# Optimization experiments

Hardware: AMD Instinct MI355X
Metric: run time of the kernel (lower is better)

## Reference

```python
import jax, jax.numpy as jnp
import numpy as np

EPS = 1e-5
NUM_HEADS = 8
TOP_K = 4

def _ln(x, s, b):
    m = x.mean(-1, keepdims=True)
    v = ((x - m) ** 2).mean(-1, keepdims=True)
    return (x - m) / jnp.sqrt(v + EPS) * s + b

def _mha(x, wq, bq, wk, bk, wv, bv, wo, bo):
    B, S, D = x.shape
    dh = D // NUM_HEADS
    q = (x @ wq + bq).reshape(B, S, NUM_HEADS, dh)
    k = (x @ wk + bk).reshape(B, S, NUM_HEADS, dh)
    v = (x @ wv + bv).reshape(B, S, NUM_HEADS, dh)
    att = jnp.einsum('bqhd,bkhd->bhqk', q, k) / np.sqrt(dh).astype(x.dtype)
    a = jax.nn.softmax(att, axis=-1)
    o = jnp.einsum('bhqk,bkhd->bqhd', a, v).reshape(B, S, D)
    return o @ wo + bo

def _moe(x, rd, ru, w1, b1, w2, b2, ws1, bs1, ws2, bs2):
    B, S, D = x.shape
    N = B * S
    E = ru.shape[-1]
    t = x.reshape(N, D)
    scores = (t @ rd) @ ru                       # [N,E] low-rank router
    probs = jax.nn.softmax(scores, axis=-1)
    tv, ti = jax.lax.top_k(probs, TOP_K)          # [N,K]
    tw = tv / tv.sum(-1, keepdims=True)           # renormalized gate weights
    oh = jax.nn.one_hot(ti, E, dtype=t.dtype)     # [N,K,E]
    gates = (oh * tw[..., None]).sum(1)           # sparse [N,E] combine weights
    h = jax.nn.gelu(jnp.einsum('nd,edh->enh', t, w1) + b1[:, None, :])
    eo = jnp.einsum('enh,ehd->end', h, w2) + b2[:, None, :]
    routed = jnp.einsum('end,ne->nd', eo, gates)
    shared = jax.nn.gelu(t @ ws1 + bs1) @ ws2 + bs2
    out = (routed + shared).reshape(B, S, D)
    # aux losses: load-balance + router z-loss
    f = oh.sum(1).mean(0)                         # mean assignments per expert
    P = probs.mean(0)
    lb = (E / TOP_K) * jnp.sum(f * P)
    z = jnp.mean(jax.nn.logsumexp(scores, axis=-1) ** 2)
    return out, lb, z

def reference(x, ln1_s, ln1_b, ln2_s, ln2_b, wq, bq, wk, bk, wv, bv, wo, bo,
              router_down, router_up, w1, b1, w2, b2, ws1, bs1, ws2, bs2, fn_s, fn_b):
    L = wq.shape[0]
    lbs, zs = [], []
    for l in range(L):
        x = x + _mha(_ln(x, ln1_s[l], ln1_b[l]), wq[l], bq[l], wk[l], bk[l],
                     wv[l], bv[l], wo[l], bo[l])
        moe_out, lb, z = _moe(_ln(x, ln2_s[l], ln2_b[l]), router_down[l], router_up[l],
                              w1[l], b1[l], w2[l], b2[l], ws1[l], bs1[l], ws2[l], bs2[l])
        x = x + moe_out
        lbs.append(lb)
        zs.append(z)
    x = _ln(x, fn_s, fn_b)
    return x, jnp.stack(lbs), jnp.stack(zs)

def setup_inputs() -> dict:
    key = jax.random.key(0)
    ks = jax.random.split(key, 16)
    L, D, E, R, H, HS, B, S = 2, 512, 32, 64, 512, 4096, 4, 1024
    w = 0.02  # init scale for weights
    return {
        'x': jax.random.normal(ks[0], (B, S, D), jnp.float32),
        'ln1_s': jnp.ones((L, D)), 'ln1_b': jnp.zeros((L, D)),
        'ln2_s': jnp.ones((L, D)), 'ln2_b': jnp.zeros((L, D)),
        'wq': jax.random.normal(ks[1], (L, D, D)) * w, 'bq': jnp.zeros((L, D)),
        'wk': jax.random.normal(ks[2], (L, D, D)) * w, 'bk': jnp.zeros((L, D)),
        'wv': jax.random.normal(ks[3], (L, D, D)) * w, 'bv': jnp.zeros((L, D)),
        'wo': jax.random.normal(ks[4], (L, D, D)) * w, 'bo': jnp.zeros((L, D)),
        'router_down': jax.random.normal(ks[5], (L, D, R)) * w,
        'router_up': jax.random.normal(ks[6], (L, R, E)) * w,
        'w1': jax.random.normal(ks[7], (L, E, D, H)) * w, 'b1': jnp.zeros((L, E, H)),
        'w2': jax.random.normal(ks[8], (L, E, H, D)) * w, 'b2': jnp.zeros((L, E, D)),
        'ws1': jax.random.normal(ks[9], (L, D, HS)) * w, 'bs1': jnp.zeros((L, HS)),
        'ws2': jax.random.normal(ks[10], (L, HS, D)) * w, 'bs2': jnp.zeros((L, D)),
        'fn_s': jnp.ones((D,)), 'fn_b': jnp.zeros((D,)),
    }
```

## Files before the change

kernel.cpp:

```cpp
#include <hip/hip_runtime.h>
#include <math.h>

#define NTOK    4096
#define DMODEL  512
#define NEXP    32
#define RRANK   64
#define HEXP    512
#define HSHARED 4096
#define SEQ     1024
#define BATCH   4
#define NHEAD   8
#define TOPK    4
#define NLAYER  2
#define QBLK    64
#define KBLK    64
#define MAXTILE 160
#define DDU     262144

typedef __attribute__((ext_vector_type(8))) short bf16x8;
typedef __attribute__((ext_vector_type(4))) float f32x4;

__device__ __forceinline__ float gelu_f(float x) {
    float t = tanhf(0.7978845608028654f * (x + 0.044715f * x * x * x));
    return 0.5f * x * (1.f + t);
}
__device__ __forceinline__ unsigned short f2bf(float f) {
    unsigned int u = __float_as_uint(f);
    u += 0x7FFFu + ((u >> 16) & 1u);
    return (unsigned short)(u >> 16);
}
__device__ __forceinline__ float bf2f(unsigned short u) {
    return __uint_as_float((unsigned int)u << 16);
}
__device__ __forceinline__ void gl_lds16(const void* g, void* l) {
    __builtin_amdgcn_global_load_lds(
        (const __attribute__((address_space(1))) void*)g,
        (__attribute__((address_space(3))) void*)l, 16, 0, 0);
}

__device__ __forceinline__ void ln_body(const float* x, const float* s, const float* b,
                                        unsigned short* outb, int rowblk) {
    int wave = threadIdx.x >> 6, lane = threadIdx.x & 63;
    int row = rowblk * 4 + wave;
    const float* xr = x + (size_t)row * DMODEL;
    float v[8];
    float sum = 0.f;
#pragma unroll
    for (int i = 0; i < 8; i++) { v[i] = xr[lane + i * 64]; sum += v[i]; }
#pragma unroll
    for (int o = 32; o; o >>= 1) sum += __shfl_xor(sum, o);
    float m = sum * (1.f / DMODEL);
    float vs = 0.f;
#pragma unroll
    for (int i = 0; i < 8; i++) { float d = v[i] - m; vs += d * d; }
#pragma unroll
    for (int o = 32; o; o >>= 1) vs += __shfl_xor(vs, o);
    float rstd = rsqrtf(vs * (1.f / DMODEL) + 1e-5f);
#pragma unroll
    for (int i = 0; i < 8; i++) {
        int c = lane + i * 64;
        outb[(size_t)row * DMODEL + c] = f2bf((v[i] - m) * rstd * s[c] + b[c]);
    }
}

template <int SK, bool MOE, int MODE, bool ROUTER = false>
__global__ __launch_bounds__(256) void reduceln_kernel(
    const float* __restrict__ pbuf, const float* __restrict__ bias,
    const unsigned short* __restrict__ eogb, const float* __restrict__ topw,
    const int* __restrict__ pos, float* __restrict__ xb,
    const float* __restrict__ s, const float* __restrict__ b,
    float* __restrict__ outf, unsigned short* __restrict__ outb,
    const float* __restrict__ rdru, float* __restrict__ rsc) {
    int wave = threadIdx.x >> 6, lane = threadIdx.x & 63;
    int row = blockIdx.x * 4 + wave;
    int cb = lane * 8;
    size_t base = (size_t)row * DMODEL + cb;
    float v[8];
    {
        float4 a0 = *(const float4*)(xb + base);
        float4 a1 = *(const float4*)(xb + base + 4);
        float4 b0 = *(const float4*)(bias + cb);
        float4 b1 = *(const float4*)(bias + cb + 4);
        v[0] = a0.x + b0.x; v[1] = a0.y + b0.y; v[2] = a0.z + b0.z; v[3] = a0.w + b0.w;
        v[4] = a1.x + b1.x; v[5] = a1.y + b1.y; v[6] = a1.z + b1.z; v[7] = a1.w + b1.w;
    }
#pragma unroll
    for (int sk = 0; sk < SK; sk++) {
        const float* p = pbuf + (size_t)sk * NTOK * DMODEL + base;
        float4 p0 = *(const float4*)p;
        float4 p1 = *(const float4*)(p + 4);
        v[0] += p0.x; v[1] += p0.y; v[2] += p0.z; v[3] += p0.w;
        v[4] += p1.x; v[5] += p1.y; v[6] += p1.z; v[7] += p1.w;
    }
    if (MOE) {
#pragma unroll
        for (int k = 0; k < TOPK; k++) {
            float w = topw[row * TOPK + k];
            bf16x8 e = *(const bf16x8*)(eogb + (size_t)pos[row * TOPK + k] * DMODEL + cb);
#pragma unroll
            for (int i = 0; i < 8; i++) v[i] += w * bf2f((unsigned short)e[i]);
        }
    }
    *(float4*)(xb + base) = make_float4(v[0], v[1], v[2], v[3]);
    *(float4*)(xb + base + 4) = make_float4(v[4], v[5], v[6], v[7]);
    float sum = 0.f;
#pragma unroll
    for (int i = 0; i < 8; i++) sum += v[i];
#pragma unroll
    for (int o = 32; o; o >>= 1) sum += __shfl_xor(sum, o);
    float m = sum * (1.f / DMODEL);
    float vs = 0.f;
#pragma unroll
    for (int i = 0; i < 8; i++) { float d = v[i] - m; vs += d * d; }
#pragma unroll
    for (int o = 32; o; o >>= 1) vs += __shfl_xor(vs, o);
    float rstd = rsqrtf(vs * (1.f / DMODEL) + 1e-5f);
    float rr[8];
#pragma unroll
    for (int i = 0; i < 8; i++) {
        int c = cb + i;
        rr[i] = (v[i] - m) * rstd * s[c] + b[c];
        if (MODE != 1) outf[(size_t)row * DMODEL + c] = rr[i];
        if (MODE != 0) outb[(size_t)row * DMODEL + c] = f2bf(rr[i]);
    }
    if (ROUTER) {
        float sc[NEXP];
#pragma unroll
        for (int e = 0; e < NEXP; e++) sc[e] = 0.f;
#pragma unroll
        for (int i = 0; i < 8; i++) {
            const float4* rp = (const float4*)(rdru + (size_t)(cb + i) * NEXP);
            float rv = rr[i];
#pragma unroll
            for (int e4 = 0; e4 < 8; e4++) {
                float4 q = rp[e4];
                sc[e4 * 4 + 0] += rv * q.x;
                sc[e4 * 4 + 1] += rv * q.y;
                sc[e4 * 4 + 2] += rv * q.z;
                sc[e4 * 4 + 3] += rv * q.w;
            }
        }
#pragma unroll
        for (int e = 0; e < NEXP; e++) {
#pragma unroll
            for (int o = 32; o; o >>= 1) sc[e] += __shfl_xor(sc[e], o);
        }
        if (lane == 0) {
            float* rp = rsc + (size_t)row * NEXP;
#pragma unroll
            for (int e = 0; e < NEXP; e++) rp[e] = sc[e];
        }
    }
}

__device__ __forceinline__ void wt_tile_body(char* ldsraw, const float* src,
                                             unsigned short* dst, int K, int N,
                                             int tx, int ty) {
    float (*tbuf)[68] = (float(*)[68])ldsraw;
    int tid = threadIdx.x;
    int k0 = ty * 64, n0 = tx * 64;
    int r = tid >> 2, cb4 = (tid & 3) * 4;
#pragma unroll
    for (int i = 0; i < 4; i++)
        *(float4*)&tbuf[r][cb4 + i * 16] = *(const float4*)(src + (size_t)(k0 + r) * N + n0 + cb4 + i * 16);
    __syncthreads();
    int g = tid & 7, nr = tid >> 3;
#pragma unroll
    for (int i = 0; i < 2; i++) {
        int n = nr + i * 32;
        bf16x8 v;
#pragma unroll
        for (int j = 0; j < 8; j++) v[j] = (short)f2bf(tbuf[g * 8 + j][n]);
        *(bf16x8*)(dst + (size_t)(n0 + n) * K + k0 + g * 8) = v;
    }
}

__device__ __forceinline__ void rdru_tile_body(char* ldsraw, const float* A,
                                               const float* W, float* C, int m0) {
    float (*Asf)[68] = (float(*)[68])ldsraw;
    float (*Wsf)[68] = (float(*)[68])(ldsraw + 4352);
    int tid = threadIdx.x;
    int ml = tid >> 2, kl = (tid & 3) << 2;
    const float* aptr = A + (size_t)(m0 + ml) * RRANK + kl;
    int kr = tid >> 4, nc = (tid & 15) << 2;
    bool wvalid = nc < NEXP;
    const float* wptr = W + (size_t)kr * NEXP + nc;
    int tm = (tid >> 4) << 2, tn = (tid & 15) << 2;
    float acc[4][4] = {{0.f}};
    for (int k0 = 0; k0 < RRANK; k0 += 16) {
        float4 av = *(const float4*)(aptr + k0);
        float4 wv = make_float4(0.f, 0.f, 0.f, 0.f);
        if (wvalid) wv = *(const float4*)(wptr + (size_t)k0 * NEXP);
        Asf[kl + 0][ml] = av.x; Asf[kl + 1][ml] = av.y;
        Asf[kl + 2][ml] = av.z; Asf[kl + 3][ml] = av.w;
        *(float4*)&Wsf[kr][nc] = wv;
        __syncthreads();
#pragma unroll
        for (int kk = 0; kk < 16; kk++) {
            float4 a4 = *(const float4*)&Asf[kk][tm];
            float4 w4 = *(const float4*)&Wsf[kk][tn];
            acc[0][0] += a4.x * w4.x; acc[0][1] += a4.x * w4.y; acc[0][2] += a4.x * w4.z; acc[0][3] += a4.x * w4.w;
            acc[1][0] += a4.y * w4.x; acc[1][1] += a4.y * w4.y; acc[1][2] += a4.y * w4.z; acc[1][3] += a4.y * w4.w;
            acc[2][0] += a4.z * w4.x; acc[2][1] += a4.z * w4.y; acc[2][2] += a4.z * w4.z; acc[2][3] += a4.z * w4.w;
            acc[3][0] += a4.w * w4.x; acc[3][1] += a4.w * w4.y; acc[3][2] += a4.w * w4.z; acc[3][3] += a4.w * w4.w;
        }
        __syncthreads();
    }
#pragma unroll
    for (int i = 0; i < 4; i++) {
        float* crow = C + (size_t)(m0 + tm + i) * NEXP;
#pragma unroll
        for (int j = 0; j < 4; j++) {
            int nn = tn + j;
            if (nn < NEXP) crow[nn] = acc[i][j];
        }
    }
}

__global__ __launch_bounds__(256) void prep0_kernel(
    const float* __restrict__ wq, const float* __restrict__ wk, const float* __restrict__ wv,
    const float* __restrict__ bq, const float* __restrict__ bk, const float* __restrict__ bv,
    unsigned short* __restrict__ wqkvt, float* __restrict__ bqkv, int* __restrict__ stats,
    const float* __restrict__ rdw, const float* __restrict__ ruw, float* __restrict__ rdru,
    const float* __restrict__ xb, const float* __restrict__ ln1_s, const float* __restrict__ ln1_b,
    unsigned short* __restrict__ hb) {
    __shared__ char lds[17408];
    int bkid = blockIdx.x;
    int tid = threadIdx.x;
    if (bkid < 192) {
        int w = bkid >> 6, t = bkid & 63;
        const float* src = (w == 0) ? wq : (w == 1 ? wk : wv);
        wt_tile_body(lds, src, wqkvt + (size_t)w * DDU, 512, 512, t & 7, t >> 3);
    } else if (bkid < 198) {
        int i = (bkid - 192) * 256 + tid;
        float val = (i < 512) ? bq[i] : (i < 1024 ? bk[i - 512] : bv[i - 1024]);
        bqkv[i] = val;
        if (i < 160) stats[i] = 0;
    } else if (bkid < 206) {
        rdru_tile_body(lds, rdw, ruw, rdru, (bkid - 198) * 64);
    } else {
        ln_body(xb, ln1_s, ln1_b, hb, bkid - 206);
    }
}

__global__ __launch_bounds__(256) void vtr_kernel(const unsigned short* __restrict__ QKV,
                                                  unsigned short* __restrict__ Vt) {
    int st = blockIdx.x, hh = blockIdx.y, bb = blockIdx.z;
    __shared__ unsigned short t[64][72];
    int r = threadIdx.x >> 3, g = threadIdx.x & 7;
#pragma unroll
    for (int i = 0; i < 2; i++) {
        int row = r + i * 32;
        bf16x8 v = *(const bf16x8*)(QKV + (size_t)(bb * SEQ + st * 64 + row) * 1536 + 1024 + hh * 64 + g * 8);
        *(bf16x8*)&t[row][g * 8] = v;
    }
    __syncthreads();
#pragma unroll
    for (int i = 0; i < 2; i++) {
        int d = r + i * 32;
        bf16x8 v;
#pragma unroll
        for (int j = 0; j < 8; j++) v[j] = (short)t[g * 8 + j][d];
        *(bf16x8*)(Vt + (size_t)((bb * NHEAD + hh) * 64 + d) * SEQ + st * 64 + g * 8) = v;
    }
}

template <bool GELU, bool GATHER, bool EXPERT, bool OUTBF16, int SK>
__device__ __forceinline__ void gemm_body(
    char* asb, char* bsb,
    unsigned int rb, unsigned int gx, unsigned int tot, int zidx,
    const unsigned short* Ab, const unsigned short* Wt,
    const float* bias, void* Cvoid, int M, int Nn, int Kk,
    const int* rowmap, const int* cntp, const int* offp, const int* tinfo) {
    constexpr int RS  = 128;
    constexpr int CH  = 8;
    constexpr int RPI = 8;
    constexpr int AIW = 4;
    constexpr int BIW = 2;
    unsigned int lg = (rb & 7) * (tot >> 3) + (rb >> 3);
    unsigned int bx = lg % gx;
    unsigned int by = lg / gx;
    int n0 = bx * 64;
    int m0;
    size_t cbase = 0;
    int kbeg = 0, kend = Kk;
    if (EXPERT) {
        int t = by;
        if (t >= tinfo[0]) return;
        int e = tinfo[1 + 2 * t];
        m0 = tinfo[2 + 2 * t];
        M = cntp[e];
        Wt += (size_t)e * Nn * Kk;
        bias += (size_t)e * Nn;
        int oe = offp[e];
        cbase = (size_t)oe * Nn;
        if (GATHER) rowmap += oe;
        else Ab += (size_t)oe * Kk;
    } else {
        m0 = by * 128;
    }
    if (SK > 1) {
        int chunk = Kk / SK;
        kbeg = zidx * chunk;
        kend = kbeg + chunk;
        cbase = (size_t)zidx * M * Nn;
    }
    int tid = threadIdx.x;
    int wave = tid >> 6, lane = tid & 63;
    int wm = wave >> 1, wn = wave & 1;
    int l15 = lane & 15, l16 = lane >> 4;
    int c16 = lane & (CH - 1);
    int ro  = lane / CH;

    const char* aptr[AIW];
    const char* bptr[BIW];
#pragma unroll
    for (int j = 0; j < AIW; j++) {
        int rloc = j * RPI + ro;
        int row = wave * 32 + rloc;
        int grow = m0 + row;
        int arow = GATHER ? rowmap[grow] : grow;
        int srcoff = ((c16 ^ (rloc & (CH - 1))) << 4);
        aptr[j] = (const char*)Ab + (((size_t)arow * Kk) << 1) + srcoff;
    }
#pragma unroll
    for (int j = 0; j < BIW; j++) {
        int rloc = j * RPI + ro;
        int row = wave * 16 + rloc;
        int srcoff = ((c16 ^ (rloc & (CH - 1))) << 4);
        bptr[j] = (const char*)Wt + (((size_t)(n0 + row) * Kk) << 1) + srcoff;
    }

    f32x4 acc[4][2];
#pragma unroll
    for (int m = 0; m < 4; m++)
#pragma unroll
        for (int n = 0; n < 2; n++)
#pragma unroll
            for (int j = 0; j < 4; j++) acc[m][n][j] = 0.f;

    for (int k0 = kbeg; k0 < kend; k0 += 64) {
        size_t kb = (size_t)k0 << 1;
#pragma unroll
        for (int j = 0; j < AIW; j++) gl_lds16(aptr[j] + kb, asb + wave * 32 * RS + j * 1024);
#pragma unroll
        for (int j = 0; j < BIW; j++) gl_lds16(bptr[j] + kb, bsb + wave * 16 * RS + j * 1024);
        __syncthreads();
#pragma unroll
        for (int kk = 0; kk < 2; kk++) {
            int k8 = kk * 4 + l16;
            bf16x8 a[4], b[2];
#pragma unroll
            for (int m = 0; m < 4; m++) {
                int row = wm * 64 + m * 16 + l15;
                a[m] = *(const bf16x8*)(asb + row * RS + ((k8 * 16) ^ ((row & (CH - 1)) << 4)));
            }
#pragma unroll
            for (int n = 0; n < 2; n++) {
                int row = wn * 32 + n * 16 + l15;
                b[n] = *(const bf16x8*)(bsb + row * RS + ((k8 * 16) ^ ((row & (CH - 1)) << 4)));
            }
#pragma unroll
            for (int m = 0; m < 4; m++)
#pragma unroll
                for (int n = 0; n < 2; n++)
                    acc[m][n] = __builtin_amdgcn_mfma_f32_16x16x32_bf16(a[m], b[n], acc[m][n], 0, 0, 0);
        }
        __syncthreads();
    }

#pragma unroll
    for (int m = 0; m < 4; m++) {
#pragma unroll
        for (int n = 0; n < 2; n++) {
            int col = n0 + wn * 32 + n * 16 + l15;
            float bv = (SK == 1 && bias) ? bias[col] : 0.f;
#pragma unroll
            for (int j = 0; j < 4; j++) {
                int row = m0 + wm * 64 + m * 16 + l16 * 4 + j;
                if (row >= M) continue;
                float val = acc[m][n][j] + bv;
                if (SK == 1 && GELU) val = gelu_f(val);
                if (SK == 1 && OUTBF16)
                    ((unsigned short*)Cvoid)[cbase + (size_t)row * Nn + col] = f2bf(val);
                else
                    ((float*)Cvoid)[cbase + (size_t)row * Nn + col] = val;
            }
        }
    }
}

template <int RIDER>
__global__ __launch_bounds__(256, 2) void qkv_kernel(
    const unsigned short* __restrict__ hb, const unsigned short* __restrict__ wqkvt,
    const float* __restrict__ bqkv, unsigned short* __restrict__ qkv_bf,
    const float* __restrict__ srcA, const float* __restrict__ srcB,
    unsigned short* __restrict__ dstA, unsigned short* __restrict__ dstB,
    int* __restrict__ stats) {
    __shared__ char lds[24576];
    unsigned int bid = blockIdx.x;
    if (bid < 768) {
        gemm_body<false, false, false, true, 1>(
            lds, lds + 16384, bid, 24, 768, 0,
            hb, wqkvt, bqkv, qkv_bf, NTOK, 1536, DMODEL, nullptr, nullptr, nullptr, nullptr);
    } else if (RIDER == 0) {
        int t = bid - 768;
        wt_tile_body(lds, srcA, dstA, 512, 512, t & 7, t >> 3);
    } else {
        unsigned int eb = bid - 768;
        if (eb < 2048) {
            int e = eb >> 6, tt = eb & 63;
            wt_tile_body(lds, srcA + (size_t)e * DDU, dstA + (size_t)e * DDU,
                         512, 512, tt & 7, tt >> 3);
        } else if (eb < 2560) {
            int t = eb - 2048;
            wt_tile_body(lds, srcB, dstB, 4096, 512, t & 7, t >> 3);
        } else {
            if (threadIdx.x < 160) stats[threadIdx.x] = 0;
        }
    }
}

__device__ __forceinline__ void attn_body(char* lds, unsigned int bid,
                                          const unsigned short* QKV,
                                          const unsigned short* Vt,
                                          unsigned short* O) {
    int qt = bid & 15, hh = (bid >> 4) & 7, bb = bid >> 7;
    char* Qs = lds;
    char* Ks = lds + 8192;
    char* Vs = lds + 16384;
    char* Ps = lds + 24576;
    int tid = threadIdx.x;
    int w = tid >> 6, l = tid & 63;
    int l15 = l & 15, l16 = l >> 4;

    {
        int r = tid >> 3, g = tid & 7;
        const unsigned short* qbase = QKV + (size_t)(bb * SEQ + qt * QBLK) * 1536 + hh * 64;
#pragma unroll
        for (int i = 0; i < 2; i++) {
            int row = r + i * 32;
            bf16x8 v = *(const bf16x8*)(qbase + (size_t)row * 1536 + g * 8);
            *(bf16x8*)(Qs + row * 128 + ((g * 16) ^ ((row & 7) << 4))) = v;
        }
    }
    f32x4 accO[4];
#pragma unroll
    for (int n = 0; n < 4; n++)
#pragma unroll
        for (int j = 0; j < 4; j++) accO[n][j] = 0.f;
    float m_r[4] = {-1e30f, -1e30f, -1e30f, -1e30f};
    float l_r[4] = {0.f, 0.f, 0.f, 0.f};

    const unsigned short* kbase = QKV + (size_t)(bb * SEQ) * 1536 + 512 + hh * 64;
    const unsigned short* vbase = Vt + (size_t)((bb * NHEAD + hh) * 64) * SEQ;

    for (int kt = 0; kt < SEQ / KBLK; kt++) {
        __syncthreads();
        {
            int r = tid >> 3, g = tid & 7;
#pragma unroll
            for (int i = 0; i < 2; i++) {
                int row = r + i * 32;
                bf16x8 kv = *(const bf16x8*)(kbase + (size_t)(kt * KBLK + row) * 1536 + g * 8);
                *(bf16x8*)(Ks + row * 128 + ((g * 16) ^ ((row & 7) << 4))) = kv;
                bf16x8 vv = *(const bf16x8*)(vbase + (size_t)row * SEQ + kt * KBLK + g * 8);
                *(bf16x8*)(Vs + row * 128 + ((g * 16) ^ ((row & 7) << 4))) = vv;
            }
        }
        __syncthreads();
        f32x4 s_acc[4];
#pragma unroll
        for (int n = 0; n < 4; n++)
#pragma unroll
            for (int j = 0; j < 4; j++) s_acc[n][j] = 0.f;
#pragma unroll
        for (int st = 0; st < 2; st++) {
            int kb = st * 64 + l16 * 16;
            int qrow = w * 16 + l15;
            bf16x8 a = *(const bf16x8*)(Qs + qrow * 128 + (kb ^ ((qrow & 7) << 4)));
#pragma unroll
            for (int n = 0; n < 4; n++) {
                int kr = n * 16 + l15;
                bf16x8 b = *(const bf16x8*)(Ks + kr * 128 + (kb ^ ((kr & 7) << 4)));
                s_acc[n] = __builtin_amdgcn_mfma_f32_16x16x32_bf16(a, b, s_acc[n], 0, 0, 0);
            }
        }
        char* pw = Ps + w * 2048;
#pragma unroll
        for (int j = 0; j < 4; j++) {
            float s0 = s_acc[0][j] * 0.125f, s1 = s_acc[1][j] * 0.125f;
            float s2 = s_acc[2][j] * 0.125f, s3 = s_acc[3][j] * 0.125f;
            float tmax = fmaxf(fmaxf(s0, s1), fmaxf(s2, s3));
#pragma unroll
            for (int o = 1; o < 16; o <<= 1) tmax = fmaxf(tmax, __shfl_xor(tmax, o));
            float mnew = fmaxf(m_r[j], tmax);
            float resc = __expf(m_r[j] - mnew);
            float p0 = __expf(s0 - mnew), p1 = __expf(s1 - mnew);
            float p2 = __expf(s2 - mnew), p3 = __expf(s3 - mnew);
            float ps = p0 + p1 + p2 + p3;
#pragma unroll
            for (int o = 1; o < 16; o <<= 1) ps += __shfl_xor(ps, o);
            l_r[j] = l_r[j] * resc + ps;
            m_r[j] = mnew;
            accO[0][j] *= resc; accO[1][j] *= resc;
            accO[2][j] *= resc; accO[3][j] *= resc;
            int prow = l16 * 4 + j;
            int sw = (prow & 7) << 4;
            *(unsigned short*)(pw + prow * 128 + ((2 * l15) ^ sw)) = f2bf(p0);
            *(unsigned short*)(pw + prow * 128 + ((2 * l15 + 32) ^ sw)) = f2bf(p1);
            *(unsigned short*)(pw + prow * 128 + ((2 * l15 + 64) ^ sw)) = f2bf(p2);
            *(unsigned short*)(pw + prow * 128 + ((2 * l15 + 96) ^ sw)) = f2bf(p3);
        }
#pragma unroll
        for (int st = 0; st < 2; st++) {
            int kb = st * 64 + l16 * 16;
            bf16x8 pa = *(const bf16x8*)(pw + l15 * 128 + (kb ^ ((l15 & 7) << 4)));
#pragma unroll
            for (int n = 0; n < 4; n++) {
                int vr = n * 16 + l15;
                bf16x8 vb = *(const bf16x8*)(Vs + vr * 128 + (kb ^ ((vr & 7) << 4)));
                accO[n] = __builtin_amdgcn_mfma_f32_16x16x32_bf16(pa, vb, accO[n], 0, 0, 0);
            }
        }
    }
    unsigned short* obase = O + (size_t)(bb * SEQ + qt * QBLK + w * 16) * DMODEL + hh * 64;
#pragma unroll
    for (int j = 0; j < 4; j++) {
        float inv = 1.f / l_r[j];
        int row = l16 * 4 + j;
#pragma unroll
        for (int n = 0; n < 4; n++)
            obase[(size_t)row * DMODEL + n * 16 + l15] = f2bf(accO[n][j] * inv);
    }
}

template <int RIDER>
__global__ __launch_bounds__(256, 2) void attn_kernel(
    const unsigned short* __restrict__ QKV, const unsigned short* __restrict__ Vt,
    unsigned short* __restrict__ O,
    const float* __restrict__ w1src, const float* __restrict__ ws1src,
    unsigned short* __restrict__ w1t, unsigned short* __restrict__ ws1t) {
    __shared__ char lds[32768];
    unsigned int bid = blockIdx.x;
    if (bid < 512) {
        attn_body(lds, bid, QKV, Vt, O);
    } else if (RIDER == 0) {
        unsigned int eb = bid - 512;
        if (eb < 2048) {
            int e = eb >> 6, tt = eb & 63;
            wt_tile_body(lds, w1src + (size_t)e * DDU, w1t + (size_t)e * DDU,
                         512, 512, tt & 7, tt >> 3);
        } else {
            int t = eb - 2048;
            wt_tile_body(lds, ws1src, ws1t, 512, 4096, t & 63, t >> 6);
        }
    }
}

template <int RIDER>
__global__ __launch_bounds__(256, 2) void op_kernel(
    const unsigned short* __restrict__ t1b, const unsigned short* __restrict__ wot,
    float* __restrict__ pbuf,
    const float* __restrict__ w2src, const float* __restrict__ ws2src,
    unsigned short* __restrict__ w2t, unsigned short* __restrict__ ws2t) {
    __shared__ char lds[24576];
    unsigned int bid = blockIdx.x;
    if (bid < 512) {
        gemm_body<false, false, false, false, 2>(
            lds, lds + 16384, bid & 255, 8, 256, bid >> 8,
            t1b, wot, nullptr, pbuf, NTOK, DMODEL, DMODEL, nullptr, nullptr, nullptr, nullptr);
    } else if (RIDER == 0) {
        unsigned int eb = bid - 512;
        if (eb < 2048) {
            int e = eb >> 6, tt = eb & 63;
            wt_tile_body(lds, w2src + (size_t)e * DDU, w2t + (size_t)e * DDU,
                         512, 512, tt & 7, tt >> 3);
        } else {
            int t = eb - 2048;
            wt_tile_body(lds, ws2src, ws2t, 4096, 512, t & 7, t >> 3);
        }
    }
}

__global__ __launch_bounds__(256, 2) void mlp1_kernel(
    const unsigned short* __restrict__ hb,
    const unsigned short* __restrict__ ws1t, const float* __restrict__ bs1,
    unsigned short* __restrict__ hidb,
    const unsigned short* __restrict__ w1t, const float* __restrict__ b1,
    unsigned short* __restrict__ ehid,
    const int* __restrict__ perm, const int* __restrict__ cnt,
    const int* __restrict__ poff, const int* __restrict__ tinfo,
    const float* __restrict__ nwq, const float* __restrict__ nwk,
    const float* __restrict__ nwv, const float* __restrict__ nwo,
    const float* __restrict__ nbq, const float* __restrict__ nbk, const float* __restrict__ nbv,
    unsigned short* __restrict__ wqkvt, unsigned short* __restrict__ wot,
    float* __restrict__ bqkv,
    const float* __restrict__ nrdw, const float* __restrict__ nruw, float* __restrict__ rdru) {
    __shared__ char lds[24576];
    unsigned int bid = blockIdx.x;
    if (bid < 2048) {
        gemm_body<true, false, false, true, 1>(
            lds, lds + 16384, bid, 64, 2048, 0,
            hb, ws1t, bs1, hidb, NTOK, HSHARED, DMODEL, nullptr, nullptr, nullptr, nullptr);
    } else if (bid < 3328) {
        gemm_body<true, true, true, true, 1>(
            lds, lds + 16384, bid - 2048, 8, 1280, 0,
            hb, w1t, b1, ehid, 0, HEXP, DMODEL, perm, cnt, poff, tinfo);
    } else {
        unsigned int eb = bid - 3328;
        if (eb < 256) {
            int w = eb >> 6, t = eb & 63;
            const float* src; unsigned short* dst;
            if (w == 0)      { src = nwq; dst = wqkvt; }
            else if (w == 1) { src = nwk; dst = wqkvt + DDU; }
            else if (w == 2) { src = nwv; dst = wqkvt + 2 * (size_t)DDU; }
            else             { src = nwo; dst = wot; }
            wt_tile_body(lds, src, dst, 512, 512, t & 7, t >> 3);
        } else if (eb < 262) {
            int i = (eb - 256) * 256 + threadIdx.x;
            float val = (i < 512) ? nbq[i] : (i < 1024 ? nbk[i - 512] : nbv[i - 1024]);
            bqkv[i] = val;
        } else {
            rdru_tile_body(lds, nrdw, nruw, rdru, (eb - 262) * 64);
        }
    }
}

__global__ __launch_bounds__(256, 2) void mlp2_kernel(
    const unsigned short* __restrict__ hidb,
    const unsigned short* __restrict__ ws2t, float* __restrict__ pbuf,
    const unsigned short* __restrict__ ehid,
    const unsigned short* __restrict__ w2t, const float* __restrict__ b2,
    unsigned short* __restrict__ eogb,
    const int* __restrict__ cnt, const int* __restrict__ poff,
    const int* __restrict__ tinfo,
    const float* __restrict__ nw1, const float* __restrict__ nws1,
    unsigned short* __restrict__ w1t, unsigned short* __restrict__ ws1t) {
    __shared__ char lds[24576];
    unsigned int bid = blockIdx.x;
    if (bid < 1024) {
        int zidx = bid >> 8;
        gemm_body<false, false, false, false, 4>(
            lds, lds + 16384, bid & 255, 8, 256, zidx,
            hidb, ws2t, nullptr, pbuf, NTOK, DMODEL, HSHARED, nullptr, nullptr, nullptr, nullptr);
    } else if (bid < 2304) {
        gemm_body<false, false, true, true, 1>(
            lds, lds + 16384, bid - 1024, 8, 1280, 0,
            ehid, w2t, b2, eogb, 0, DMODEL, HEXP, nullptr, cnt, poff, tinfo);
    } else {
        unsigned int eb = bid - 2304;
        if (eb < 2048) {
            int e = eb >> 6, tt = eb & 63;
            wt_tile_body(lds, nw1 + (size_t)e * DDU, w1t + (size_t)e * DDU,
                         512, 512, tt & 7, tt >> 3);
        } else {
            int t = eb - 2048;
            wt_tile_body(lds, nws1, ws1t, 512, 4096, t & 63, t >> 6);
        }
    }
}

__global__ __launch_bounds__(256) void router_topk(const float* __restrict__ rsc,
                                                   float* __restrict__ topw,
                                                   int* __restrict__ topi,
                                                   int* __restrict__ cnt,
                                                   float* __restrict__ sumP,
                                                   float* __restrict__ zacc,
                                                   int* __restrict__ done,
                                                   int* __restrict__ poff,
                                                   int* __restrict__ tinfo,
                                                   int* __restrict__ perm,
                                                   float* __restrict__ out_aux, int l) {
    __shared__ float wP[4][NEXP];
    __shared__ int wC[4][NEXP];
    __shared__ float wZ[4];
    __shared__ int amLast;
    int tid = threadIdx.x;
    int wv = tid >> 6, lane = tid & 63;
    int n = blockIdx.x * 256 + tid;
    float sc[NEXP];
    float mx = -1e30f;
#pragma unroll
    for (int e = 0; e < NEXP; e++) { sc[e] = rsc[n * NEXP + e]; mx = fmaxf(mx, sc[e]); }
    float se = 0.f;
#pragma unroll
    for (int e = 0; e < NEXP; e++) { sc[e] = expf(sc[e] - mx); se += sc[e]; }
    float invse = 1.f / se;
    float lse = mx + logf(se);
    float z = lse * lse;
#pragma unroll
    for (int o = 32; o; o >>= 1) z += __shfl_xor(z, o);
    if (lane == 0) wZ[wv] = z;
#pragma unroll
    for (int e = 0; e < NEXP; e++) {
        float pv = sc[e] * invse;
#pragma unroll
        for (int o = 32; o; o >>= 1) pv += __shfl_xor(pv, o);
        if (lane == 0) wP[wv][e] = pv;
    }
    float tv[TOPK]; int ti[TOPK];
#pragma unroll
    for (int k = 0; k < TOPK; k++) {
        float best = -1.f; int bi = 0;
#pragma unroll
        for (int e = 0; e < NEXP; e++) {
            if (sc[e] > best) { best = sc[e]; bi = e; }
        }
        tv[k] = best * invse; ti[k] = bi; sc[bi] = -1.f;
    }
    float s4 = tv[0] + tv[1] + tv[2] + tv[3];
#pragma unroll
    for (int k = 0; k < TOPK; k++) {
        topw[n * TOPK + k] = tv[k] / s4;
        topi[n * TOPK + k] = ti[k];
    }
#pragma unroll
    for (int e = 0; e < NEXP; e++) {
        unsigned long long b0 = __ballot(ti[0] == e);
        unsigned long long b1 = __ballot(ti[1] == e);
        unsigned long long b2 = __ballot(ti[2] == e);
        unsigned long long b3 = __ballot(ti[3] == e);
        if (lane == 0)
            wC[wv][e] = __popcll(b0) + __popcll(b1) + __popcll(b2) + __popcll(b3);
    }
    __syncthreads();
    if (tid < NEXP) {
        atomicAdd(&sumP[tid], wP[0][tid] + wP[1][tid] + wP[2][tid] + wP[3][tid]);
        atomicAdd(&cnt[tid], wC[0][tid] + wC[1][tid] + wC[2][tid] + wC[3][tid]);
    }
    if (tid == 0) atomicAdd(zacc, wZ[0] + wZ[1] + wZ[2] + wZ[3]);
    __syncthreads();
    __threadfence();
    if (tid == 0) amLast = (atomicAdd(done, 1) == (int)gridDim.x - 1);
    __syncthreads();
    if (amLast && tid < 64) {
        __threadfence();
        int laneid = tid;
        int c = (laneid < NEXP) ? atomicAdd(&cnt[laneid], 0) : 0;
        int nt = (c + 127) >> 7;
        int x = nt;
#pragma unroll
        for (int o = 1; o < 32; o <<= 1) {
            int y = __shfl_up(x, o);
            if (laneid >= o) x += y;
        }
        int excl = x - nt;
        if (laneid < NEXP) {
            poff[laneid] = excl * 128;
            for (int i = 0; i < nt; i++) {
                tinfo[1 + 2 * (excl + i)] = laneid;
                tinfo[2 + 2 * (excl + i)] = i * 128;
            }
            for (int i = c; i < nt * 128; i++) perm[excl * 128 + i] = 0;
        }
        float sp = (laneid < NEXP) ? atomicAdd(&sumP[laneid], 0.f) : 0.f;
        float lb = (laneid < NEXP) ? ((float)c / (float)NTOK) * (sp / (float)NTOK) : 0.f;
#pragma unroll
        for (int o = 32; o; o >>= 1) lb += __shfl_xor(lb, o);
        if (laneid == 31) {
            tinfo[0] = x;
            out_aux[l] = lb * (float)NEXP / (float)TOPK;
            out_aux[NLAYER + l] = atomicAdd(zacc, 0.f) / (float)NTOK;
        }
    }
}

__global__ __launch_bounds__(256) void scatter_kernel(const int* __restrict__ topi,
                                                      const int* __restrict__ poff,
                                                      int* __restrict__ cursor,
                                                      int* __restrict__ perm,
                                                      int* __restrict__ pos) {
    __shared__ int lcnt[NEXP];
    __shared__ int lbase[NEXP];
    if (threadIdx.x < NEXP) lcnt[threadIdx.x] = 0;
    __syncthreads();
    int i = blockIdx.x * 256 + threadIdx.x;
    int e = topi[i];
    int lr = atomicAdd(&lcnt[e], 1);
    __syncthreads();
    if (threadIdx.x < NEXP && lcnt[threadIdx.x] > 0)
        lbase[threadIdx.x] = atomicAdd(&cursor[threadIdx.x], lcnt[threadIdx.x]);
    __syncthreads();
    int g = poff[e] + lbase[e] + lr;
    perm[g] = i >> 2;
    pos[i] = g;
}

extern "C" void kernel_launch(void* const* d_in, const int* in_sizes, int n_in,
                              void* d_out, int out_size, void* d_ws, size_t ws_size,
                              hipStream_t stream) {
    (void)in_sizes; (void)n_in; (void)out_size; (void)ws_size;
    const float* x_in  = (const float*)d_in[0];
    const float* ln1_s = (const float*)d_in[1];
    const float* ln1_b = (const float*)d_in[2];
    const float* ln2_s = (const float*)d_in[3];
    const float* ln2_b = (const float*)d_in[4];
    const float* wq = (const float*)d_in[5];
    const float* bq = (const float*)d_in[6];
    const float* wk = (const float*)d_in[7];
    const float* bk = (const float*)d_in[8];
    const float* wv = (const float*)d_in[9];
    const float* bv = (const float*)d_in[10];
    const float* wo = (const float*)d_in[11];
    const float* bo = (const float*)d_in[12];
    const float* rdw = (const float*)d_in[13];
    const float* ruw = (const float*)d_in[14];
    const float* w1 = (const float*)d_in[15];
    const float* b1 = (const float*)d_in[16];
    const float* w2 = (const float*)d_in[17];
    const float* b2 = (const float*)d_in[18];
    const float* ws1 = (const float*)d_in[19];
    const float* bs1 = (const float*)d_in[20];
    const float* ws2 = (const float*)d_in[21];
    const float* bs2 = (const float*)d_in[22];
    const float* fn_s = (const float*)d_in[23];
    const float* fn_b = (const float*)d_in[24];

    float* ws = (float*)d_ws;
    const size_t ND = (size_t)NTOK * DMODEL;
    const size_t PADROWS = (size_t)MAXTILE * 128;
    size_t o = 0;
    float* xb  = ws + o; o += ND;
    unsigned short* hb     = (unsigned short*)(ws + o); o += ND / 2;
    unsigned short* qkv_bf = (unsigned short*)(ws + o); o += (size_t)NTOK * 1536 / 2;
    unsigned short* vT     = (unsigned short*)(ws + o); o += ND / 2;
    unsigned short* t1b    = (unsigned short*)(ws + o); o += ND / 2;
    unsigned short* hidb   = (unsigned short*)(ws + o); o += (size_t)NTOK * HSHARED / 2;
    unsigned short* ehid   = (unsigned short*)(ws + o); o += PADROWS * HEXP / 2;
    unsigned short* eogb   = (unsigned short*)(ws + o); o += PADROWS * DMODEL / 2;
    float* pbuf = ws + o; o += 4 * ND;
    float* rdru = ws + o; o += (size_t)DMODEL * NEXP;
    float* rsc  = ws + o; o += (size_t)NTOK * NEXP;
    float* topw = ws + o; o += (size_t)NTOK * TOPK;
    float* bqkv = ws + o; o += 1536;
    int* topi = (int*)(ws + o); o += (size_t)NTOK * TOPK;
    int* pos  = (int*)(ws + o); o += (size_t)NTOK * TOPK;
    int* perm = (int*)(ws + o); o += PADROWS;
    int* stats = (int*)(ws + o); o += 256;
    int* tinfo = (int*)(ws + o); o += 512;
    int* cnt = stats;
    int* cursor = stats + 32;
    int* poff = stats + 64;
    float* sumP = (float*)(stats + 96);
    float* zacc = sumP + 32;
    int* done = stats + 129;
    unsigned short* wbf = (unsigned short*)(ws + o);
    unsigned short* wqkvt = wbf;
    unsigned short* wot  = wqkvt + 3 * (size_t)DDU;
    unsigned short* w1t  = wot + DDU;
    unsigned short* w2t  = w1t + (size_t)NEXP * DDU;
    unsigned short* ws1t = w2t + (size_t)NEXP * DDU;
    unsigned short* ws2t = ws1t + (size_t)DMODEL * HSHARED;

    float* out_x = (float*)d_out;
    float* out_aux = out_x + ND;

    hipMemcpyAsync(xb, x_in, ND * sizeof(float), hipMemcpyDeviceToDevice, stream);

    dim3 blk(256);

    for (int l = 0; l < NLAYER; l++) {
        const size_t DD = (size_t)DMODEL * DMODEL;
        bool hasNext = (l + 1 < NLAYER);
        int lnx = hasNext ? (l + 1) : l;
        if (l == 0) {
            prep0_kernel<<<1230, blk, 0, stream>>>(
                wq, wk, wv, bq, bk, bv, wqkvt, bqkv, stats,
                rdw, ruw, rdru, xb, ln1_s, ln1_b, hb);
            qkv_kernel<0><<<832, blk, 0, stream>>>(
                hb, wqkvt, bqkv, qkv_bf, wo, nullptr, wot, nullptr, nullptr);
        } else {
            qkv_kernel<1><<<3329, blk, 0, stream>>>(
                hb, wqkvt, bqkv, qkv_bf,
                w2 + (size_t)l * NEXP * DD, ws2 + (size_t)l * HSHARED * DMODEL,
                w2t, ws2t, stats);
        }
        vtr_kernel<<<dim3(SEQ / 64, NHEAD, BATCH), blk, 0, stream>>>(qkv_bf, vT);
        if (l == 0)
            attn_kernel<0><<<3072, blk, 0, stream>>>(qkv_bf, vT, t1b, w1, ws1, w1t, ws1t);
        else
            attn_kernel<1><<<512, blk, 0, stream>>>(qkv_bf, vT, t1b, nullptr, nullptr, nullptr, nullptr);
        if (l == 0)
            op_kernel<0><<<3072, blk, 0, stream>>>(t1b, wot, pbuf, w2, ws2, w2t, ws2t);
        else
            op_kernel<1><<<512, blk, 0, stream>>>(t1b, wot, pbuf, nullptr, nullptr, nullptr, nullptr);
        reduceln_kernel<2, false, 1, true><<<NTOK / 4, blk, 0, stream>>>(
            pbuf, bo + l * DMODEL, nullptr, nullptr, nullptr, xb,
            ln2_s + l * DMODEL, ln2_b + l * DMODEL, nullptr, hb, rdru, rsc);
        router_topk<<<NTOK / 256, blk, 0, stream>>>(
            rsc, topw, topi, cnt, sumP, zacc, done, poff, tinfo, perm, out_aux, l);
        scatter_kernel<<<NTOK * TOPK / 256, blk, 0, stream>>>(topi, poff, cursor, perm, pos);
        int ln1g = hasNext ? 3598 : 3328;
        mlp1_kernel<<<ln1g, blk, 0, stream>>>(
            hb, ws1t, bs1 + (size_t)l * HSHARED, hidb,
            w1t, b1 + (size_t)l * NEXP * HEXP, ehid,
            perm, cnt, poff, tinfo,
            wq + (size_t)lnx * DD, wk + (size_t)lnx * DD,
            wv + (size_t)lnx * DD, wo + (size_t)lnx * DD,
            bq + (size_t)lnx * DMODEL, bk + (size_t)lnx * DMODEL, bv + (size_t)lnx * DMODEL,
            wqkvt, wot, bqkv,
            rdw + (size_t)lnx * DMODEL * RRANK, ruw + (size_t)lnx * RRANK * NEXP, rdru);
        int ln2g = hasNext ? 4864 : 2304;
        mlp2_kernel<<<ln2g, blk, 0, stream>>>(
            hidb, ws2t, pbuf,
            ehid, w2t, b2 + (size_t)l * NEXP * DMODEL, eogb,
            cnt, poff, tinfo,
            w1 + (size_t)lnx * NEXP * DD, ws1 + (size_t)lnx * DMODEL * HSHARED,
            w1t, ws1t);
        if (hasNext) {
            reduceln_kernel<4, true, 1, false><<<NTOK / 4, blk, 0, stream>>>(
                pbuf, bs2 + l * DMODEL, eogb, topw, pos, xb,
                ln1_s + (l + 1) * DMODEL, ln1_b + (l + 1) * DMODEL, nullptr, hb, nullptr, nullptr);
        } else {
            reduceln_kernel<4, true, 0, false><<<NTOK / 4, blk, 0, stream>>>(
                pbuf, bs2 + l * DMODEL, eogb, topw, pos, xb,
                fn_s, fn_b, out_x, nullptr, nullptr, nullptr);
        }
    }
}
```

Measured before the change: 510.5 us.

## Fuse V transpose into QKV GEMM epilogue and use sigmoid-form GELU

Removes the separate vtr_kernel launch. The QKV GEMM epilogue now also writes the V columns into the transposed vT buffer directly. Separately, the tanh GELU is rewritten as x*sigmoid(2u) using __expf and a hardware reciprocal, which is cheaper than tanhf. The transposed writes are scattered 2-byte stores with poor coalescing, which may cost more than the dropped launch and its read of V. The fast reciprocal also slightly changes numerics.

```diff
diff --git a/kernel.cpp b/kernel.cpp
--- a/kernel.cpp
+++ b/kernel.cpp
@@ -21,8 +21,8 @@
 typedef __attribute__((ext_vector_type(4))) float f32x4;
 
 __device__ __forceinline__ float gelu_f(float x) {
-    float t = tanhf(0.7978845608028654f * (x + 0.044715f * x * x * x));
-    return 0.5f * x * (1.f + t);
+    float u = 1.5957691216057308f * (x + 0.044715f * x * x * x);
+    return x * __builtin_amdgcn_rcpf(1.f + __expf(-u));
 }
 __device__ __forceinline__ unsigned short f2bf(float f) {
     unsigned int u = __float_as_uint(f);
@@ -243,35 +243,14 @@
     }
 }
 
-__global__ __launch_bounds__(256) void vtr_kernel(const unsigned short* __restrict__ QKV,
-                                                  unsigned short* __restrict__ Vt) {
-    int st = blockIdx.x, hh = blockIdx.y, bb = blockIdx.z;
-    __shared__ unsigned short t[64][72];
-    int r = threadIdx.x >> 3, g = threadIdx.x & 7;
-#pragma unroll
-    for (int i = 0; i < 2; i++) {
-        int row = r + i * 32;
-        bf16x8 v = *(const bf16x8*)(QKV + (size_t)(bb * SEQ + st * 64 + row) * 1536 + 1024 + hh * 64 + g * 8);
-        *(bf16x8*)&t[row][g * 8] = v;
-    }
-    __syncthreads();
-#pragma unroll
-    for (int i = 0; i < 2; i++) {
-        int d = r + i * 32;
-        bf16x8 v;
-#pragma unroll
-        for (int j = 0; j < 8; j++) v[j] = (short)t[g * 8 + j][d];
-        *(bf16x8*)(Vt + (size_t)((bb * NHEAD + hh) * 64 + d) * SEQ + st * 64 + g * 8) = v;
-    }
-}
-
-template <bool GELU, bool GATHER, bool EXPERT, bool OUTBF16, int SK>
+template <bool GELU, bool GATHER, bool EXPERT, bool OUTBF16, int SK, bool VT = false>
 __device__ __forceinline__ void gemm_body(
     char* asb, char* bsb,
     unsigned int rb, unsigned int gx, unsigned int tot, int zidx,
     const unsigned short* Ab, const unsigned short* Wt,
     const float* bias, void* Cvoid, int M, int Nn, int Kk,
-    const int* rowmap, const int* cntp, const int* offp, const int* tinfo) {
+    const int* rowmap, const int* cntp, const int* offp, const int* tinfo,
+    unsigned short* vtout = nullptr) {
     constexpr int RS  = 128;
     constexpr int CH  = 8;
     constexpr int RPI = 8;
@@ -381,10 +360,18 @@
                 if (row >= M) continue;
                 float val = acc[m][n][j] + bv;
                 if (SK == 1 && GELU) val = gelu_f(val);
-                if (SK == 1 && OUTBF16)
-                    ((unsigned short*)Cvoid)[cbase + (size_t)row * Nn + col] = f2bf(val);
-                else
+                if (SK == 1 && OUTBF16) {
+                    unsigned short obf = f2bf(val);
+                    ((unsigned short*)Cvoid)[cbase + (size_t)row * Nn + col] = obf;
+                    if (VT && col >= 1024) {
+                        int cc = col - 1024;
+                        int bb = row >> 10;
+                        int s  = row & (SEQ - 1);
+                        vtout[(size_t)(bb * 512 + cc) * SEQ + s] = obf;
+                    }
+                } else {
                     ((float*)Cvoid)[cbase + (size_t)row * Nn + col] = val;
+                }
             }
         }
     }
@@ -394,15 +381,17 @@
 __global__ __launch_bounds__(256, 2) void qkv_kernel(
     const unsigned short* __restrict__ hb, const unsigned short* __restrict__ wqkvt,
     const float* __restrict__ bqkv, unsigned short* __restrict__ qkv_bf,
+    unsigned short* __restrict__ vtout,
     const float* __restrict__ srcA, const float* __restrict__ srcB,
     unsigned short* __restrict__ dstA, unsigned short* __restrict__ dstB,
     int* __restrict__ stats) {
     __shared__ char lds[24576];
     unsigned int bid = blockIdx.x;
     if (bid < 768) {
-        gemm_body<false, false, false, true, 1>(
+        gemm_body<false, false, false, true, 1, true>(
             lds, lds + 16384, bid, 24, 768, 0,
-            hb, wqkvt, bqkv, qkv_bf, NTOK, 1536, DMODEL, nullptr, nullptr, nullptr, nullptr);
+            hb, wqkvt, bqkv, qkv_bf, NTOK, 1536, DMODEL, nullptr, nullptr, nullptr, nullptr,
+            vtout);
     } else if (RIDER == 0) {
         int t = bid - 768;
         wt_tile_body(lds, srcA, dstA, 512, 512, t & 7, t >> 3);
@@ -869,14 +858,13 @@
                 wq, wk, wv, bq, bk, bv, wqkvt, bqkv, stats,
                 rdw, ruw, rdru, xb, ln1_s, ln1_b, hb);
             qkv_kernel<0><<<832, blk, 0, stream>>>(
-                hb, wqkvt, bqkv, qkv_bf, wo, nullptr, wot, nullptr, nullptr);
+                hb, wqkvt, bqkv, qkv_bf, vT, wo, nullptr, wot, nullptr, nullptr);
         } else {
             qkv_kernel<1><<<3329, blk, 0, stream>>>(
-                hb, wqkvt, bqkv, qkv_bf,
+                hb, wqkvt, bqkv, qkv_bf, vT,
                 w2 + (size_t)l * NEXP * DD, ws2 + (size_t)l * HSHARED * DMODEL,
                 w2t, ws2t, stats);
         }
-        vtr_kernel<<<dim3(SEQ / 64, NHEAD, BATCH), blk, 0, stream>>>(qkv_bf, vT);
         if (l == 0)
             attn_kernel<0><<<3072, blk, 0, stream>>>(qkv_bf, vT, t1b, w1, ws1, w1t, ws1t);
         else
```

Result: faster. 485.0 us (-5.0%).
